# Performance work log

Measured on AMD Instinct MI355X. Metric: run time of the kernel, lower is better.

The kernel has to match this reference:

```python
import jax, jax.numpy as jnp
import numpy as np

N, D, T = 8192, 512, 200000


def _pairwise_sq_dists(x):
    # dist[i,j] = ||x_i - x_j||^2, clamped at 0 like the torch version
    sq = jnp.sum(x * x, axis=1)
    d = sq[:, None] + sq[None, :] - 2.0 * (x @ x.T)
    return jnp.maximum(d, 0.0)


def setup_inputs() -> dict:
    key = jax.random.key(0)
    kx, ky, kt = jax.random.split(key, 3)
    x = jax.random.normal(kx, (N, D), dtype=jnp.float32)
    y = jax.random.normal(ky, (N, D), dtype=jnp.float32)
    norm_s = jnp.ones((1,), dtype=jnp.float32)  # NormalizationLayer learned scale
    triplets = jax.random.randint(kt, (T, 3), 0, N, dtype=jnp.int32)
    return {"x": x, "y": y, "norm_s": norm_s, "triplets": triplets}


def reference(x, y, norm_s, triplets):
    # NormalizationLayer on y (pre_layer is None so x passes through)
    y_n = norm_s * y / jnp.linalg.norm(y, axis=1, keepdims=True)

    d_img = _pairwise_sq_dists(x)
    d_txt = _pairwise_sq_dists(y_n)

    i, j, k = triplets[:, 0], triplets[:, 1], triplets[:, 2]
    # log(1 + exp(d_ij - d_ik)) == softplus
    loss_img = jnp.mean(jax.nn.softplus(d_img[i, j] - d_img[i, k]))
    loss_txt = jnp.mean(jax.nn.softplus(d_txt[i, j] - d_txt[i, k]))
    return (loss_img + loss_txt)[None]  # shape (1,), matching torch output
```

## Files before the change

kernel.cpp:

```cpp
#include <hip/hip_runtime.h>
#include <math.h>

#define NROWS 8192
#define DDIM  512
#define NTRIP 200000
#define CHUNK 16
#define MAXCH 4
#define BINCAP 64
#define NCHUNKS (NROWS * MAXCH)
#define NBLK (NCHUNKS / 4)
#define ROWU 128

#define SXQ 25.6f
#define DSX (1.0f / (SXQ * SXQ))

__device__ __forceinline__ float wave_sum_all(float v) {
    #pragma unroll
    for (int off = 32; off > 0; off >>= 1) v += __shfl_xor(v, off, 64);
    return v;
}

__device__ __forceinline__ int dot4i8(int a, int b, int c) {
#if __has_builtin(__builtin_amdgcn_sdot4)
    return __builtin_amdgcn_sdot4(a, b, c, false);
#else
    #pragma unroll
    for (int e = 0; e < 4; ++e)
        c += (int)(signed char)(a >> (8 * e)) * (int)(signed char)(b >> (8 * e));
    return c;
#endif
}

__device__ __forceinline__ int dot32i(const uint4 ra, const uint4 rb,
                                      const uint4 ca, const uint4 cb) {
    int p = 0;
    p = dot4i8((int)ra.x, (int)ca.x, p);
    p = dot4i8((int)ra.y, (int)ca.y, p);
    p = dot4i8((int)ra.z, (int)ca.z, p);
    p = dot4i8((int)ra.w, (int)ca.w, p);
    p = dot4i8((int)rb.x, (int)cb.x, p);
    p = dot4i8((int)rb.y, (int)cb.y, p);
    p = dot4i8((int)rb.z, (int)cb.z, p);
    p = dot4i8((int)rb.w, (int)cb.w, p);
    return p;
}

__device__ __forceinline__ unsigned int packi8(float a, float b, float c, float d) {
    const int qa = (int)rintf(a), qb = (int)rintf(b);
    const int qc = (int)rintf(c), qd = (int)rintf(d);
    return (unsigned int)((qa & 255) | ((qb & 255) << 8) |
                          ((qc & 255) << 16) | ((qd & 255) << 24));
}

__device__ __forceinline__ float softplus_fast(float z) {
    return fmaxf(z, 0.0f) + __logf(1.0f + __expf(-fabsf(z)));
}

__global__ __launch_bounds__(256) void prep_kernel(
    const float* __restrict__ x, const float* __restrict__ y,
    const float* __restrict__ norm_s,
    const int* __restrict__ trip, int* __restrict__ count,
    int2* __restrict__ slots,
    unsigned int* __restrict__ xq, unsigned int* __restrict__ yq,
    float2* __restrict__ sq)
{
    const int tid = blockIdx.x * 256 + threadIdx.x;
    if (tid < NTRIP) {
        const int i = trip[3*tid], j = trip[3*tid+1], k = trip[3*tid+2];
        const int c = atomicAdd(&count[i], 1);
        if (c < BINCAP) slots[((size_t)i << 6) + c] = (int2){j, k};
    }

    const int row  = blockIdx.x * 4 + (threadIdx.x >> 6);
    const int lane = threadIdx.x & 63;
    const float4* xr = (const float4*)(x + (size_t)row * DDIM);
    const float4* yr = (const float4*)(y + (size_t)row * DDIM);
    const float4 x0 = xr[lane], x1 = xr[lane + 64];
    const float4 y0 = yr[lane], y1 = yr[lane + 64];

    float sy = y0.x*y0.x + y0.y*y0.y + y0.z*y0.z + y0.w*y0.w
             + y1.x*y1.x + y1.y*y1.y + y1.z*y1.z + y1.w*y1.w;
    sy = wave_sum_all(sy);
    const float us = 127.0f / sqrtf(sy);

    #define QX(v) fminf(fmaxf((v) * SXQ, -127.0f), 127.0f)
    const unsigned int ux0 = packi8(QX(x0.x), QX(x0.y), QX(x0.z), QX(x0.w));
    const unsigned int ux1 = packi8(QX(x1.x), QX(x1.y), QX(x1.z), QX(x1.w));
    #undef QX
    const unsigned int uy0 = packi8(y0.x*us, y0.y*us, y0.z*us, y0.w*us);
    const unsigned int uy1 = packi8(y1.x*us, y1.y*us, y1.z*us, y1.w*us);

    int pxi = 0, pyi = 0;
    pxi = dot4i8((int)ux0, (int)ux0, pxi); pxi = dot4i8((int)ux1, (int)ux1, pxi);
    pyi = dot4i8((int)uy0, (int)uy0, pyi); pyi = dot4i8((int)uy1, (int)uy1, pyi);
    const float sxs = wave_sum_all((float)pxi);
    const float sys = wave_sum_all((float)pyi);

    const float ns  = norm_s[0];
    const float dsy = ns * ns * (1.0f / 16129.0f);

    ((uint2*)(xq + (size_t)row * ROWU))[lane] = (uint2){ux0, ux1};
    ((uint2*)(yq + (size_t)row * ROWU))[lane] = (uint2){uy0, uy1};
    if (lane == 0) sq[row] = (float2){sxs * DSX, sys * dsy};
}

__global__ __launch_bounds__(256) void trip_kernel(
    const unsigned int* __restrict__ xq, const unsigned int* __restrict__ yq,
    const float* __restrict__ norm_s,
    const float2* __restrict__ sq, const int* __restrict__ count,
    const int2* __restrict__ slots, float* __restrict__ bpart)
{
    const int tid  = threadIdx.x;
    const int lane = tid & 63;
    const int wv   = tid >> 6;
    const int chunk = blockIdx.x * 4 + wv;
    const int c    = chunk >> 13;
    const int bin  = chunk & (NROWS - 1);

    float acc = 0.0f;
    int n = count[bin];
    n = __builtin_amdgcn_readfirstlane(n < BINCAP ? n : BINCAP);
    int m = n - c * CHUNK;
    if (m > 0) {
        if (m > CHUNK) m = CHUNK;

        const int  s     = lane & 15;
        const bool isK   = (lane & 16) != 0;
        const bool isTxt = (lane & 32) != 0;
        const unsigned int* base = isTxt ? yq : xq;
        const float ns = norm_s[0];
        const float dscale = isTxt ? (ns * ns * (1.0f / 16129.0f)) : DSX;

        const uint4* irow = ((const uint4*)(base + (size_t)bin * ROWU)) + (s << 1);
        const uint4 ca = irow[0], cb = irow[1];

        const float2 sqi = sq[bin];
        const float sq_self = isTxt ? sqi.y : sqi.x;
        const int2* bs = slots + ((size_t)bin << 6) + c * CHUNK;

        const int2 myslot = bs[s];
        const int jsl = myslot.x, ksl = myslot.y;

        int t = 0;
        for (; t + 4 <= m; t += 4) {
            int jj[4], kk[4];
            #pragma unroll
            for (int u = 0; u < 4; ++u) {
                jj[u] = __builtin_amdgcn_readfirstlane(__shfl(jsl, t + u, 64));
                kk[u] = __builtin_amdgcn_readfirstlane(__shfl(ksl, t + u, 64));
            }
            uint4 ra[4], rb[4];
            #pragma unroll
            for (int u = 0; u < 4; ++u) {
                const int r = isK ? kk[u] : jj[u];
                const uint4* rp = ((const uint4*)(base + (size_t)r * ROWU)) + (s << 1);
                ra[u] = rp[0]; rb[u] = rp[1];
            }
            float sq_r[4];
            #pragma unroll
            for (int u = 0; u < 4; ++u) {
                const float2 sqj = sq[jj[u]];
                const float2 sqk = sq[kk[u]];
                sq_r[u] = isTxt ? (isK ? sqk.y : sqj.y) : (isK ? sqk.x : sqj.x);
            }
            float dist[4];
            #pragma unroll
            for (int u = 0; u < 4; ++u) {
                int p = dot32i(ra[u], rb[u], ca, cb);
                #pragma unroll
                for (int off = 1; off < 16; off <<= 1) p += __shfl_xor(p, off, 64);
                dist[u] = fmaxf(sq_self + sq_r[u] - 2.0f * (float)p * dscale, 0.0f);
            }
            #pragma unroll
            for (int u = 0; u < 4; ++u) {
                const float z = dist[u] - __shfl_xor(dist[u], 16, 64);
                acc += isK ? 0.0f : softplus_fast(z);
            }
        }
        for (; t < m; ++t) {
            const int j0 = __builtin_amdgcn_readfirstlane(__shfl(jsl, t, 64));
            const int k0 = __builtin_amdgcn_readfirstlane(__shfl(ksl, t, 64));
            const int r = isK ? k0 : j0;
            const uint4* rp = ((const uint4*)(base + (size_t)r * ROWU)) + (s << 1);
            int p = dot32i(rp[0], rp[1], ca, cb);
            #pragma unroll
            for (int off = 1; off < 16; off <<= 1) p += __shfl_xor(p, off, 64);
            const float2 sqj = sq[j0];
            const float2 sqk = sq[k0];
            const float sq_r = isTxt ? (isK ? sqk.y : sqj.y) : (isK ? sqk.x : sqj.x);
            const float dist = fmaxf(sq_self + sq_r - 2.0f * (float)p * dscale, 0.0f);
            const float z = dist - __shfl_xor(dist, 16, 64);
            acc += isK ? 0.0f : softplus_fast(z);
        }
    }

    acc = wave_sum_all(acc);
    __shared__ float red[4];
    if (lane == 0) red[wv] = acc;
    __syncthreads();
    if (tid == 0) bpart[blockIdx.x] = red[0] + red[1] + red[2] + red[3];
}

__global__ __launch_bounds__(256) void reduce_kernel(
    const float* __restrict__ bpart, float* __restrict__ out)
{
    const float4* bp4 = (const float4*)bpart;
    float s = 0.0f;
    #pragma unroll
    for (int it = 0; it < NBLK / 4 / 256; ++it) {
        const float4 v = bp4[it * 256 + threadIdx.x];
        s += (v.x + v.y) + (v.z + v.w);
    }
    s = wave_sum_all(s);
    __shared__ float red[4];
    const int wv = threadIdx.x >> 6, lane = threadIdx.x & 63;
    if (lane == 0) red[wv] = s;
    __syncthreads();
    if (threadIdx.x == 0)
        out[0] = (red[0] + red[1] + red[2] + red[3])
                 * (1.0f / (16.0f * (float)NTRIP));
}

extern "C" void kernel_launch(void* const* d_in, const int* in_sizes, int n_in,
                              void* d_out, int out_size, void* d_ws, size_t ws_size,
                              hipStream_t stream) {
    const float* x      = (const float*)d_in[0];
    const float* y      = (const float*)d_in[1];
    const float* norm_s = (const float*)d_in[2];
    const int*   trip   = (const int*)d_in[3];

    unsigned int* xq    = (unsigned int*)d_ws;
    unsigned int* yq    = xq + (size_t)NROWS * ROWU;
    float2*       sq    = (float2*)(yq + (size_t)NROWS * ROWU);
    int*          count = (int*)(sq + NROWS);
    float*        bpart = (float*)(count + NROWS);
    int2*         slots = (int2*)(bpart + NBLK);

    (void)hipMemsetAsync(count, 0, sizeof(int) * NROWS, stream);
    prep_kernel<<<NROWS / 4, 256, 0, stream>>>(x, y, norm_s, trip, count, slots,
                                               xq, yq, sq);
    trip_kernel<<<NBLK, 256, 0, stream>>>(xq, yq, norm_s, (const float2*)sq,
                                          count, slots, bpart);
    reduce_kernel<<<1, 256, 0, stream>>>(bpart, (float*)d_out);
}
```

Before: 129.7 us.

## Split image/text across blocks by XCD and process two triplets per wave

Each block now handles only the image or only the text modality, chosen by blockIdx modulo 8. Blocks landing on XCDs 0-3 take image rows and blocks on XCDs 4-7 take text rows, so each XCD's L2 holds only one quantized matrix. Within a wave the two 32-lane halves now process different triplets, so twice as many blocks are launched, each doing half the work per chunk. The row indices become per-half vector values rather than wave-uniform scalars, which may cost scalar-load efficiency. A masked tail handles odd counts.

```diff
diff --git a/kernel.cpp b/kernel.cpp
--- a/kernel.cpp
+++ b/kernel.cpp
@@ -8,7 +8,7 @@
 #define MAXCH 4
 #define BINCAP 64
 #define NCHUNKS (NROWS * MAXCH)
-#define NBLK (NCHUNKS / 4)
+#define NBLK2 (NCHUNKS / 2)
 #define ROWU 128
 
 #define SXQ 25.6f
@@ -113,7 +113,11 @@
     const int tid  = threadIdx.x;
     const int lane = tid & 63;
     const int wv   = tid >> 6;
-    const int chunk = blockIdx.x * 4 + wv;
+    const int b    = blockIdx.x;
+    const int xcdm = b & 7;
+    const bool isTxt = xcdm >= 4;
+    const int bq   = (b >> 3) * 4 + (xcdm & 3);
+    const int chunk = bq * 4 + wv;
     const int c    = chunk >> 13;
     const int bin  = chunk & (NROWS - 1);
 
@@ -124,9 +128,9 @@
     if (m > 0) {
         if (m > CHUNK) m = CHUNK;
 
-        const int  s     = lane & 15;
-        const bool isK   = (lane & 16) != 0;
-        const bool isTxt = (lane & 32) != 0;
+        const int  s    = lane & 15;
+        const bool isK  = (lane & 16) != 0;
+        const int  half = lane >> 5;
         const unsigned int* base = isTxt ? yq : xq;
         const float ns = norm_s[0];
         const float dscale = isTxt ? (ns * ns * (1.0f / 16129.0f)) : DSX;
@@ -142,44 +146,72 @@
         const int jsl = myslot.x, ksl = myslot.y;
 
         int t = 0;
-        for (; t + 4 <= m; t += 4) {
-            int jj[4], kk[4];
-            #pragma unroll
-            for (int u = 0; u < 4; ++u) {
-                jj[u] = __builtin_amdgcn_readfirstlane(__shfl(jsl, t + u, 64));
-                kk[u] = __builtin_amdgcn_readfirstlane(__shfl(ksl, t + u, 64));
+        for (; t + 8 <= m; t += 8) {
+            int jp[4], kp[4];
+            #pragma unroll
+            for (int v = 0; v < 4; ++v) {
+                const int tt = t + 2 * v + half;
+                jp[v] = __shfl(jsl, tt, 64);
+                kp[v] = __shfl(ksl, tt, 64);
             }
             uint4 ra[4], rb[4];
             #pragma unroll
-            for (int u = 0; u < 4; ++u) {
-                const int r = isK ? kk[u] : jj[u];
+            for (int v = 0; v < 4; ++v) {
+                const int r = isK ? kp[v] : jp[v];
                 const uint4* rp = ((const uint4*)(base + (size_t)r * ROWU)) + (s << 1);
-                ra[u] = rp[0]; rb[u] = rp[1];
+                ra[v] = rp[0]; rb[v] = rp[1];
             }
             float sq_r[4];
             #pragma unroll
-            for (int u = 0; u < 4; ++u) {
-                const float2 sqj = sq[jj[u]];
-                const float2 sqk = sq[kk[u]];
-                sq_r[u] = isTxt ? (isK ? sqk.y : sqj.y) : (isK ? sqk.x : sqj.x);
-            }
-            float dist[4];
-            #pragma unroll
-            for (int u = 0; u < 4; ++u) {
-                int p = dot32i(ra[u], rb[u], ca, cb);
+            for (int v = 0; v < 4; ++v) {
+                const float2 sqj = sq[jp[v]];
+                const float2 sqk = sq[kp[v]];
+                sq_r[v] = isTxt ? (isK ? sqk.y : sqj.y) : (isK ? sqk.x : sqj.x);
+            }
+            #pragma unroll
+            for (int v = 0; v < 4; ++v) {
+                int p = dot32i(ra[v], rb[v], ca, cb);
                 #pragma unroll
                 for (int off = 1; off < 16; off <<= 1) p += __shfl_xor(p, off, 64);
-                dist[u] = fmaxf(sq_self + sq_r[u] - 2.0f * (float)p * dscale, 0.0f);
-            }
-            #pragma unroll
-            for (int u = 0; u < 4; ++u) {
-                const float z = dist[u] - __shfl_xor(dist[u], 16, 64);
+                const float dist = fmaxf(sq_self + sq_r[v] - 2.0f * (float)p * dscale, 0.0f);
+                const float z = dist - __shfl_xor(dist, 16, 64);
                 acc += isK ? 0.0f : softplus_fast(z);
             }
         }
-        for (; t < m; ++t) {
-            const int j0 = __builtin_amdgcn_readfirstlane(__shfl(jsl, t, 64));
-            const int k0 = __builtin_amdgcn_readfirstlane(__shfl(ksl, t, 64));
+        for (; t + 4 <= m; t += 4) {
+            int jp[2], kp[2];
+            #pragma unroll
+            for (int v = 0; v < 2; ++v) {
+                const int tt = t + 2 * v + half;
+                jp[v] = __shfl(jsl, tt, 64);
+                kp[v] = __shfl(ksl, tt, 64);
+            }
+            uint4 ra[2], rb[2];
+            #pragma unroll
+            for (int v = 0; v < 2; ++v) {
+                const int r = isK ? kp[v] : jp[v];
+                const uint4* rp = ((const uint4*)(base + (size_t)r * ROWU)) + (s << 1);
+                ra[v] = rp[0]; rb[v] = rp[1];
+            }
+            #pragma unroll
+            for (int v = 0; v < 2; ++v) {
+                int p = dot32i(ra[v], rb[v], ca, cb);
+                #pragma unroll
+                for (int off = 1; off < 16; off <<= 1) p += __shfl_xor(p, off, 64);
+                const float2 sqj = sq[jp[v]];
+                const float2 sqk = sq[kp[v]];
+                const float sq_r = isTxt ? (isK ? sqk.y : sqj.y) : (isK ? sqk.x : sqj.x);
+                const float dist = fmaxf(sq_self + sq_r - 2.0f * (float)p * dscale, 0.0f);
+                const float z = dist - __shfl_xor(dist, 16, 64);
+                acc += isK ? 0.0f : softplus_fast(z);
+            }
+        }
+        for (; t < m; t += 2) {
+            const int tt  = t + half;
+            const bool ok = tt < m;
+            const int ttc = ok ? tt : (m - 1);
+            const int j0 = __shfl(jsl, ttc, 64);
+            const int k0 = __shfl(ksl, ttc, 64);
             const int r = isK ? k0 : j0;
             const uint4* rp = ((const uint4*)(base + (size_t)r * ROWU)) + (s << 1);
             int p = dot32i(rp[0], rp[1], ca, cb);
@@ -190,7 +222,7 @@
             const float sq_r = isTxt ? (isK ? sqk.y : sqj.y) : (isK ? sqk.x : sqj.x);
             const float dist = fmaxf(sq_self + sq_r - 2.0f * (float)p * dscale, 0.0f);
             const float z = dist - __shfl_xor(dist, 16, 64);
-            acc += isK ? 0.0f : softplus_fast(z);
+            acc += (!isK && ok) ? softplus_fast(z) : 0.0f;
         }
     }
 
@@ -207,7 +239,7 @@
     const float4* bp4 = (const float4*)bpart;
     float s = 0.0f;
     #pragma unroll
-    for (int it = 0; it < NBLK / 4 / 256; ++it) {
+    for (int it = 0; it < NBLK2 / 4 / 256; ++it) {
         const float4 v = bp4[it * 256 + threadIdx.x];
         s += (v.x + v.y) + (v.z + v.w);
     }
@@ -234,12 +266,12 @@
     float2*       sq    = (float2*)(yq + (size_t)NROWS * ROWU);
     int*          count = (int*)(sq + NROWS);
     float*        bpart = (float*)(count + NROWS);
-    int2*         slots = (int2*)(bpart + NBLK);
+    int2*         slots = (int2*)(bpart + NBLK2);
 
     (void)hipMemsetAsync(count, 0, sizeof(int) * NROWS, stream);
     prep_kernel<<<NROWS / 4, 256, 0, stream>>>(x, y, norm_s, trip, count, slots,
                                                xq, yq, sq);
-    trip_kernel<<<NBLK, 256, 0, stream>>>(xq, yq, norm_s, (const float2*)sq,
-                                          count, slots, bpart);
+    trip_kernel<<<NBLK2, 256, 0, stream>>>(xq, yq, norm_s, (const float2*)sq,
+                                           count, slots, bpart);
     reduce_kernel<<<1, 256, 0, stream>>>(bpart, (float*)d_out);
 }
```

New measurement: 136.1 us. 1.05x slower.
